# Performance work log

Measured on AMD Instinct MI355X. Metric: run time of the kernel, lower is better.

Reference implementation:

```python
import jax, jax.numpy as jnp
import numpy as np

GRID, RC, RD, FEAT, HID, PE = 300, 48, 16, 27, 128, 2
B, S = 4096, 128


def _grid_sample(img, grid):
    # img: (G,C,H,W); grid: (G,B,S,2) with (x=width, y=height) in [-1,1]
    # bilinear, align_corners=True (matches torch F.grid_sample defaults used here)
    G, C, H, W = img.shape
    x = (grid[..., 0] + 1.0) * 0.5 * (W - 1)  # (G,B,S)
    y = (grid[..., 1] + 1.0) * 0.5 * (H - 1)
    x0f, y0f = jnp.floor(x), jnp.floor(y)
    x0 = jnp.clip(x0f, 0, W - 1).astype(jnp.int32)
    y0 = jnp.clip(y0f, 0, H - 1).astype(jnp.int32)
    x1 = jnp.clip(x0 + 1, 0, W - 1)
    y1 = jnp.clip(y0 + 1, 0, H - 1)
    wx = (x - x0f)[:, None]  # (G,1,B,S)
    wy = (y - y0f)[:, None]

    def gather(im, yi, xi):  # im (C,H,W), yi/xi (B,S) -> (C,B,S)
        return im[:, yi, xi]

    g = jax.vmap(gather)
    v00 = g(img, y0, x0)
    v01 = g(img, y0, x1)
    v10 = g(img, y1, x0)
    v11 = g(img, y1, x1)
    return (v00 * (1 - wy) * (1 - wx) + v01 * (1 - wy) * wx
            + v10 * wy * (1 - wx) + v11 * wy * wx)  # (G,C,B,S)


def _vm(vectors, matrices, pos):
    # pos: (B,S,3) -> (B,S,3*R)
    b, s = pos.shape[0], pos.shape[1]
    mat_coord = jnp.stack([jnp.stack([pos[..., (i + 1) % 3], pos[..., (i + 2) % 3]], -1)
                           for i in range(3)], 0)  # (3,B,S,2)
    zero = jnp.zeros_like(pos[..., 0])
    vec_coord = jnp.stack([jnp.stack([pos[..., i], zero], -1) for i in range(3)], 0)
    m = _grid_sample(matrices, mat_coord)  # (3,R,B,S)
    v = _grid_sample(vectors, vec_coord)   # (3,R,B,S)
    return (m * v).transpose(2, 3, 0, 1).reshape(b, s, -1)


_COEFFS = (2.0 ** np.linspace(0.0, PE - 1, PE)) * np.pi  # [pi, 2pi]


def _pe(x):
    parts = []
    for c in _COEFFS:
        parts.append(jnp.sin(c * x))
        parts.append(jnp.cos(c * x))
    return jnp.concatenate(parts, -1)


def setup_inputs() -> dict:
    key = jax.random.key(0)
    ks = jax.random.split(key, 12)
    x = jax.random.uniform(ks[0], (B, S, 6), dtype=jnp.float32) * 2.0 - 1.0
    vmc_vec = jax.random.normal(ks[1], (3, RC, GRID, 1), dtype=jnp.float32) * 0.1
    vmc_mat = jax.random.normal(ks[2], (3, RC, GRID, GRID), dtype=jnp.float32) * 0.1
    vmd_vec = jax.random.normal(ks[3], (3, RD, GRID, 1), dtype=jnp.float32) * 0.1
    vmd_mat = jax.random.normal(ks[4], (3, RD, GRID, GRID), dtype=jnp.float32) * 0.1
    feat_w = jax.random.normal(ks[5], (FEAT, 3 * RC), dtype=jnp.float32) / np.sqrt(3 * RC)
    din = (1 + 2 * PE) * (3 + FEAT)  # 150
    w1 = jax.random.normal(ks[6], (HID, din), dtype=jnp.float32) / np.sqrt(din)
    b1 = jnp.zeros((HID,), jnp.float32)
    w2 = jax.random.normal(ks[7], (HID, HID), dtype=jnp.float32) / np.sqrt(HID)
    b2 = jnp.zeros((HID,), jnp.float32)
    w3 = jax.random.normal(ks[8], (3, HID), dtype=jnp.float32) / np.sqrt(HID)
    b3 = jnp.zeros((3,), jnp.float32)
    return {"x": x, "vmc_vec": vmc_vec, "vmc_mat": vmc_mat, "vmd_vec": vmd_vec,
            "vmd_mat": vmd_mat, "feat_w": feat_w, "w1": w1, "b1": b1,
            "w2": w2, "b2": b2, "w3": w3, "b3": b3}


def reference(x, vmc_vec, vmc_mat, vmd_vec, vmd_mat, feat_w, w1, b1, w2, b2, w3, b3):
    pos = x[..., :3]
    dirn = x[..., 3:]
    feature = jnp.einsum('bsk,fk->bsf', _vm(vmc_vec, vmc_mat, pos), feat_w)  # (B,S,27)
    mlp_in = jnp.concatenate([feature, dirn, _pe(feature), _pe(dirn)], -1)  # (B,S,150)
    h = jax.nn.relu(jnp.einsum('bsi,hi->bsh', mlp_in, w1) + b1)
    h = jax.nn.relu(jnp.einsum('bsi,hi->bsh', h, w2) + b2)
    color = jax.nn.sigmoid(jnp.einsum('bsi,oi->bso', h, w3) + b3)  # (B,S,3)
    density = jax.nn.relu(jnp.sum(_vm(vmd_vec, vmd_mat, pos), -1, keepdims=True))
    return jnp.concatenate([color, density], -1)  # (B,S,4)
```

## Files before the change

kernel.cpp:

```cpp
#include <hip/hip_runtime.h>
#include <stdint.h>

typedef unsigned int u32;
typedef _Float16 f16;
typedef __attribute__((ext_vector_type(8))) _Float16 f16x8;
typedef __attribute__((ext_vector_type(4))) float f32x4;
typedef __attribute__((ext_vector_type(2))) float f32x2;

#define XMS 168
#define HS  136

#define WOFF_WEFF 0u
#define WOFF_W1SW 10240u
#define WOFF_W2SW 51200u
#define WOFF_W3SW 83968u
#define WOFF_VD   88064u
#define WOFF_TM   131072u
#define WS_NEED   17411072u

#define TBL_SCALE 64.0f
#define TBL_INV   (1.0f/64.0f)

__global__ void prep_k(const float* __restrict__ feat_w,
                       const float* __restrict__ vmc_vec,
                       const float* __restrict__ vmd_vec,
                       const float* __restrict__ w1,
                       const float* __restrict__ w2,
                       const float* __restrict__ w3,
                       f16* __restrict__ Weff, f16* __restrict__ W1sw,
                       f16* __restrict__ W2sw, f16* __restrict__ W3sw,
                       float* __restrict__ vd)
{
  const int N_WEFF = 5120, N_W1 = 20480, N_W2 = 16384, N_W3 = 2048, N_VD = 48;
  const int total = N_WEFF + N_W1 + N_W2 + N_W3 + N_VD;
  for (int t = blockIdx.x*blockDim.x + threadIdx.x; t < total; t += gridDim.x*blockDim.x){
    if (t < N_WEFF){
      int kb = t >> 10, n = (t >> 5) & 31, kk = t & 31, k = kb*32 + kk;
      float v = 0.f;
      if (n < 27 && k < 144)
        v = feat_w[n*144 + k] * 0.5f*(vmc_vec[k*300+149] + vmc_vec[k*300+150]) * TBL_INV;
      Weff[t] = (f16)v;
    } else if (t < N_WEFF + N_W1){
      int u = t - N_WEFF;
      int kb = u >> 12, n = (u >> 5) & 127, kk = u & 31, k = kb*32 + kk;
      W1sw[u] = (f16)((k < 150) ? w1[n*150 + k] : 0.f);
    } else if (t < N_WEFF + N_W1 + N_W2){
      int u = t - N_WEFF - N_W1;
      int kb = u >> 12, n = (u >> 5) & 127, kk = u & 31, k = kb*32 + kk;
      W2sw[u] = (f16)w2[n*128 + k];
    } else if (t < N_WEFF + N_W1 + N_W2 + N_W3){
      int u = t - N_WEFF - N_W1 - N_W2;
      int kb = u >> 9, n = (u >> 5) & 15, kk = u & 31, k = kb*32 + kk;
      W3sw[u] = (f16)((n < 3) ? w3[n*128 + k] : 0.f);
    } else {
      int k = t - N_WEFF - N_W1 - N_W2 - N_W3;
      vd[k] = 0.5f*(vmd_vec[k*300+149] + vmd_vec[k*300+150]) * TBL_INV;
    }
  }
}

__global__ void pack_feat_k(const float* __restrict__ src, u32* __restrict__ dst)
{
  __shared__ float tile[48*304];
  int i = blockIdx.x / 300, y = blockIdx.x % 300;
  const float* sp = src + (size_t)i*48*90000 + (size_t)y*300;
  for (int t = threadIdx.x; t < 48*300; t += 256){
    int r = t / 300, x = t - r*300;
    tile[r*304 + x] = sp[(size_t)r*90000 + x] * TBL_SCALE;
  }
  __syncthreads();
  u32* dp = dst + (size_t)(i*300 + y)*300*16;
  for (int t = threadIdx.x; t < 300*12; t += 256){
    int x = t / 12, cg = t - x*12;
    int c = cg*4;
    u32 v = __builtin_amdgcn_cvt_pk_fp8_f32(tile[c*304+x],     tile[(c+1)*304+x], 0, false);
    v     = __builtin_amdgcn_cvt_pk_fp8_f32(tile[(c+2)*304+x], tile[(c+3)*304+x], v, true);
    dp[x*16 + cg] = v;
  }
}

__global__ void pack_dens_k(const float* __restrict__ src, u32* __restrict__ dst)
{
  __shared__ float tile[16*304];
  int i = blockIdx.x / 300, y = blockIdx.x % 300;
  const float* sp = src + (size_t)i*16*90000 + (size_t)y*300;
  for (int t = threadIdx.x; t < 16*300; t += 256){
    int r = t / 300, x = t - r*300;
    tile[r*304 + x] = sp[(size_t)r*90000 + x] * TBL_SCALE;
  }
  __syncthreads();
  u32* dp = dst + (size_t)(i*300 + y)*300*16;
  for (int t = threadIdx.x; t < 300*4; t += 256){
    int x = t / 4, cg = t - x*4;
    int c = cg*4;
    u32 v = __builtin_amdgcn_cvt_pk_fp8_f32(tile[c*304+x],     tile[(c+1)*304+x], 0, false);
    v     = __builtin_amdgcn_cvt_pk_fp8_f32(tile[(c+2)*304+x], tile[(c+3)*304+x], v, true);
    dp[x*16 + 12 + cg] = v;
  }
}

__device__ __forceinline__ void decode16(uint4 q, float* o){
  f32x2 t;
  t = __builtin_amdgcn_cvt_pk_f32_fp8(q.x, false); o[0]=t[0];  o[1]=t[1];
  t = __builtin_amdgcn_cvt_pk_f32_fp8(q.x, true ); o[2]=t[0];  o[3]=t[1];
  t = __builtin_amdgcn_cvt_pk_f32_fp8(q.y, false); o[4]=t[0];  o[5]=t[1];
  t = __builtin_amdgcn_cvt_pk_f32_fp8(q.y, true ); o[6]=t[0];  o[7]=t[1];
  t = __builtin_amdgcn_cvt_pk_f32_fp8(q.z, false); o[8]=t[0];  o[9]=t[1];
  t = __builtin_amdgcn_cvt_pk_f32_fp8(q.z, true ); o[10]=t[0]; o[11]=t[1];
  t = __builtin_amdgcn_cvt_pk_f32_fp8(q.w, false); o[12]=t[0]; o[13]=t[1];
  t = __builtin_amdgcn_cvt_pk_f32_fp8(q.w, true ); o[14]=t[0]; o[15]=t[1];
}

__global__ __launch_bounds__(256, 3)
void main_k(const float* __restrict__ xin,
            const f16* __restrict__ WeffSw, const f16* __restrict__ W1sw,
            const f16* __restrict__ W2sw, const f16* __restrict__ W3sw,
            const float* __restrict__ vd,
            const uint4* __restrict__ Tm,
            const float* __restrict__ b1v, const float* __restrict__ b2v,
            const float* __restrict__ b3v, float* __restrict__ out)
{
  __shared__ __align__(16) f16 bufA[64*XMS];
  __shared__ __align__(16) f16 bufB[64*XMS];
  __shared__ float dLds[192];

  const int tid = threadIdx.x;
  const int l = tid & 63;
  const int w = tid >> 6;
  const size_t nidx = (size_t)blockIdx.x*64 + l;

  const float* xp = xin + nidx*6;
  float p0 = xp[0], p1 = xp[1], p2 = xp[2];
  float d0 = xp[3], d1 = xp[4], d2 = xp[5];

  if (w < 3){
    float cx = (w==0)? p1 : ((w==1)? p2 : p0);
    float cy = (w==0)? p2 : ((w==1)? p0 : p1);
    float fx = (cx+1.f)*0.5f*299.f, fy = (cy+1.f)*0.5f*299.f;
    float x0f = floorf(fx), y0f = floorf(fy);
    int x0 = min(max((int)x0f,0),299), y0 = min(max((int)y0f,0),299);
    int x1 = min(x0+1,299), y1 = min(y0+1,299);
    float wx = fx-x0f, wy = fy-y0f;
    float w11 = wx*wy, w10 = wy - w11, w01 = wx - w11, w00 = 1.f - wx - wy + w11;

    const uint4* Tb = Tm + (size_t)w*90000*4;
    const uint4* r00 = Tb + (size_t)(y0*300+x0)*4;
    const uint4* r01 = Tb + (size_t)(y0*300+x1)*4;
    const uint4* r10 = Tb + (size_t)(y1*300+x0)*4;
    const uint4* r11 = Tb + (size_t)(y1*300+x1)*4;
    uint4 qa[4], qb[4], qc[4], qd[4];
#pragma unroll
    for (int c4=0;c4<4;++c4){ qa[c4]=r00[c4]; qb[c4]=r01[c4]; qc[c4]=r10[c4]; qd[c4]=r11[c4]; }

    float vdw[16];
#pragma unroll
    for (int j=0;j<16;++j) vdw[j] = vd[w*16 + j];

    f16* dstrow = bufA + l*XMS + w*48;
    float dacc = 0.f;
#pragma unroll
    for (int c4=0;c4<4;++c4){
      float A[16],B[16],C[16],D[16];
      decode16(qa[c4],A); decode16(qb[c4],B); decode16(qc[c4],C); decode16(qd[c4],D);
      if (c4 < 3){
        f16x8 o0, o1;
#pragma unroll
        for (int j=0;j<8;++j)
          o0[j] = (f16)(w00*A[j] + w01*B[j] + w10*C[j] + w11*D[j]);
#pragma unroll
        for (int j=0;j<8;++j)
          o1[j] = (f16)(w00*A[8+j] + w01*B[8+j] + w10*C[8+j] + w11*D[8+j]);
        *(f16x8*)(dstrow + c4*16)     = o0;
        *(f16x8*)(dstrow + c4*16 + 8) = o1;
      } else {
#pragma unroll
        for (int j=0;j<16;++j)
          dacc += (w00*A[j] + w01*B[j] + w10*C[j] + w11*D[j]) * vdw[j];
      }
    }
    dLds[w*64 + l] = dacc;
  } else {
    f16x8 z = 0;
    *(f16x8*)(bufA + l*XMS + 144) = z;
    *(f16x8*)(bufA + l*XMS + 152) = z;
  }
  __syncthreads();

  const int tr = l & 15;
  const int ko = (l >> 4) * 8;

  {
    if (w == 3){
      float ds = dLds[l] + dLds[64 + l] + dLds[128 + l];
      out[nidx*4 + 3] = fmaxf(ds, 0.f);
    }
    f32x4 fa0 = {0.f,0.f,0.f,0.f}, fa1 = {0.f,0.f,0.f,0.f};
    const f16* Arow = bufA + (w*16 + tr)*XMS + ko;
#pragma unroll
    for (int kb=0; kb<5; ++kb){
      f16x8 a  = *(const f16x8*)(Arow + kb*32);
      f16x8 b0 = *(const f16x8*)(WeffSw + (size_t)(kb*32 + tr)*32 + ko);
      f16x8 b1 = *(const f16x8*)(WeffSw + (size_t)(kb*32 + 16 + tr)*32 + ko);
      fa0 = __builtin_amdgcn_mfma_f32_16x16x32_f16(a, b0, fa0, 0,0,0);
      fa1 = __builtin_amdgcn_mfma_f32_16x16x32_f16(a, b1, fa1, 0,0,0);
    }
    const int sbase = w*16 + (l>>4)*4;
#pragma unroll
    for (int nb=0; nb<2; ++nb){
      int f = nb*16 + tr;
      if (f < 27){
#pragma unroll
        for (int r=0;r<4;++r){
          float fv = nb ? fa1[r] : fa0[r];
          f16* Xr = bufB + (sbase + r)*XMS;
          Xr[f] = (f16)fv;
          float a1 = 3.14159265358979f*fv;
          float a2 = 6.28318530717959f*fv;
          Xr[30+f]  = (f16)__sinf(a1);
          Xr[57+f]  = (f16)__cosf(a1);
          Xr[84+f]  = (f16)__sinf(a2);
          Xr[111+f] = (f16)__cosf(a2);
        }
      }
    }
    if (w == 0){
      f16* Xr = bufB + l*XMS;
      Xr[27]=(f16)d0; Xr[28]=(f16)d1; Xr[29]=(f16)d2;
      float dv[3]={d0,d1,d2};
#pragma unroll
      for (int j=0;j<3;++j){
        float a1=3.14159265358979f*dv[j], a2=6.28318530717959f*dv[j];
        Xr[138+j]=(f16)__sinf(a1);
        Xr[141+j]=(f16)__cosf(a1);
        Xr[144+j]=(f16)__sinf(a2);
        Xr[147+j]=(f16)__cosf(a2);
      }
#pragma unroll
      for (int j=150;j<160;++j) Xr[j]=(f16)0.f;
    }
  }
  __syncthreads();

  {
    f32x4 acc[4][2];
#pragma unroll
    for (int m=0;m<4;++m){ acc[m][0]=(f32x4){0.f,0.f,0.f,0.f}; acc[m][1]=(f32x4){0.f,0.f,0.f,0.f}; }
    const int n0 = w*32 + tr;
#pragma unroll
    for (int kb=0; kb<5; ++kb){
      f16x8 b0 = *(const f16x8*)(W1sw + (size_t)(kb*128 + n0)*32 + ko);
      f16x8 b1 = *(const f16x8*)(W1sw + (size_t)(kb*128 + n0 + 16)*32 + ko);
#pragma unroll
      for (int m=0;m<4;++m){
        f16x8 a = *(const f16x8*)(bufB + (m*16 + tr)*XMS + kb*32 + ko);
        acc[m][0] = __builtin_amdgcn_mfma_f32_16x16x32_f16(a, b0, acc[m][0], 0,0,0);
        acc[m][1] = __builtin_amdgcn_mfma_f32_16x16x32_f16(a, b1, acc[m][1], 0,0,0);
      }
    }
    float bb0 = b1v[n0], bb1 = b1v[n0+16];
    f16* H1 = bufA;
#pragma unroll
    for (int m=0;m<4;++m){
#pragma unroll
      for (int r=0;r<4;++r){
        int ss = m*16 + (l>>4)*4 + r;
        H1[ss*HS + n0]      = (f16)fmaxf(acc[m][0][r] + bb0, 0.f);
        H1[ss*HS + n0 + 16] = (f16)fmaxf(acc[m][1][r] + bb1, 0.f);
      }
    }
  }
  __syncthreads();

  {
    f32x4 acc[4][2];
#pragma unroll
    for (int m=0;m<4;++m){ acc[m][0]=(f32x4){0.f,0.f,0.f,0.f}; acc[m][1]=(f32x4){0.f,0.f,0.f,0.f}; }
    const int n0 = w*32 + tr;
    const f16* H1 = bufA;
#pragma unroll
    for (int kb=0; kb<4; ++kb){
      f16x8 b0 = *(const f16x8*)(W2sw + (size_t)(kb*128 + n0)*32 + ko);
      f16x8 b1 = *(const f16x8*)(W2sw + (size_t)(kb*128 + n0 + 16)*32 + ko);
#pragma unroll
      for (int m=0;m<4;++m){
        f16x8 a = *(const f16x8*)(H1 + (m*16 + tr)*HS + kb*32 + ko);
        acc[m][0] = __builtin_amdgcn_mfma_f32_16x16x32_f16(a, b0, acc[m][0], 0,0,0);
        acc[m][1] = __builtin_amdgcn_mfma_f32_16x16x32_f16(a, b1, acc[m][1], 0,0,0);
      }
    }
    float bb0 = b2v[n0], bb1 = b2v[n0+16];
    f16* H2 = bufB;
#pragma unroll
    for (int m=0;m<4;++m){
#pragma unroll
      for (int r=0;r<4;++r){
        int ss = m*16 + (l>>4)*4 + r;
        H2[ss*HS + n0]      = (f16)fmaxf(acc[m][0][r] + bb0, 0.f);
        H2[ss*HS + n0 + 16] = (f16)fmaxf(acc[m][1][r] + bb1, 0.f);
      }
    }
  }
  __syncthreads();

  {
    f32x4 acc = {0.f,0.f,0.f,0.f};
    const f16* H2 = bufB;
#pragma unroll
    for (int kb=0; kb<4; ++kb){
      f16x8 a = *(const f16x8*)(H2 + (w*16 + tr)*HS + kb*32 + ko);
      f16x8 b = *(const f16x8*)(W3sw + (size_t)(kb*16 + tr)*32 + ko);
      acc = __builtin_amdgcn_mfma_f32_16x16x32_f16(a, b, acc, 0,0,0);
    }
    if (tr < 3){
      float bb = b3v[tr];
#pragma unroll
      for (int r=0;r<4;++r){
        int ss = w*16 + (l>>4)*4 + r;
        float c = acc[r] + bb;
        out[((size_t)blockIdx.x*64 + ss)*4 + tr] = 1.f/(1.f + __expf(-c));
      }
    }
  }
}

extern "C" void kernel_launch(void* const* d_in, const int* in_sizes, int n_in,
                              void* d_out, int out_size, void* d_ws, size_t ws_size,
                              hipStream_t stream)
{
  const float* xin     = (const float*)d_in[0];
  const float* vmc_vec = (const float*)d_in[1];
  const float* vmc_mat = (const float*)d_in[2];
  const float* vmd_vec = (const float*)d_in[3];
  const float* vmd_mat = (const float*)d_in[4];
  const float* feat_w  = (const float*)d_in[5];
  const float* w1      = (const float*)d_in[6];
  const float* b1      = (const float*)d_in[7];
  const float* w2      = (const float*)d_in[8];
  const float* b2      = (const float*)d_in[9];
  const float* w3      = (const float*)d_in[10];
  const float* b3      = (const float*)d_in[11];
  float* out = (float*)d_out;

  char* ws = (char*)d_ws;
  f16*   Weff = (f16*)(ws + WOFF_WEFF);
  f16*   W1sw = (f16*)(ws + WOFF_W1SW);
  f16*   W2sw = (f16*)(ws + WOFF_W2SW);
  f16*   W3sw = (f16*)(ws + WOFF_W3SW);
  float* vd   = (float*)(ws + WOFF_VD);
  u32*   Tm   = (u32*)(ws + WOFF_TM);

  prep_k<<<64, 256, 0, stream>>>(feat_w, vmc_vec, vmd_vec, w1, w2, w3,
                                 Weff, W1sw, W2sw, W3sw, vd);
  pack_feat_k<<<900, 256, 0, stream>>>(vmc_mat, Tm);
  pack_dens_k<<<900, 256, 0, stream>>>(vmd_mat, Tm);

  main_k<<<8192, 256, 0, stream>>>(xin, Weff, W1sw, W2sw, W3sw, vd,
                                   (const uint4*)Tm, b1, b2, b3, out);
}
```

Measured before the change: 222.2 us.

## Shrink LDS footprint by reusing one buffer and raise occupancy to four blocks

Merges the two large shared-memory staging buffers into one input buffer plus a smaller hidden-activation buffer. The MLP input is now built in place over the gathered features, which is safe because each wave only reads and writes its own 16 rows. Together with launch bounds raised to 4 blocks per CU, this aims to fit more blocks per CU so more latency from the random table gathers is hidden. Direction loads and their encoding are spread across all four waves instead of one, and a scheduling barrier orders the in-place overwrite. The tighter register budget risks spills.

```diff
diff --git a/kernel.cpp b/kernel.cpp
--- a/kernel.cpp
+++ b/kernel.cpp
@@ -111,7 +111,7 @@
   t = __builtin_amdgcn_cvt_pk_f32_fp8(q.w, true ); o[14]=t[0]; o[15]=t[1];
 }
 
-__global__ __launch_bounds__(256, 3)
+__global__ __launch_bounds__(256, 4)
 void main_k(const float* __restrict__ xin,
             const f16* __restrict__ WeffSw, const f16* __restrict__ W1sw,
             const f16* __restrict__ W2sw, const f16* __restrict__ W3sw,
@@ -120,8 +120,8 @@
             const float* __restrict__ b1v, const float* __restrict__ b2v,
             const float* __restrict__ b3v, float* __restrict__ out)
 {
-  __shared__ __align__(16) f16 bufA[64*XMS];
-  __shared__ __align__(16) f16 bufB[64*XMS];
+  __shared__ __align__(16) f16 buf[64*XMS];
+  __shared__ __align__(16) f16 bufH[64*HS];
   __shared__ float dLds[192];
 
   const int tid = threadIdx.x;
@@ -131,7 +131,12 @@
 
   const float* xp = xin + nidx*6;
   float p0 = xp[0], p1 = xp[1], p2 = xp[2];
-  float d0 = xp[3], d1 = xp[4], d2 = xp[5];
+
+  float dd0=0.f, dd1=0.f, dd2=0.f;
+  if (l < 16){
+    const float* dp = xin + ((size_t)blockIdx.x*64 + w*16 + l)*6 + 3;
+    dd0 = dp[0]; dd1 = dp[1]; dd2 = dp[2];
+  }
 
   if (w < 3){
     float cx = (w==0)? p1 : ((w==1)? p2 : p0);
@@ -156,7 +161,7 @@
 #pragma unroll
     for (int j=0;j<16;++j) vdw[j] = vd[w*16 + j];
 
-    f16* dstrow = bufA + l*XMS + w*48;
+    f16* dstrow = buf + l*XMS + w*48;
     float dacc = 0.f;
 #pragma unroll
     for (int c4=0;c4<4;++c4){
@@ -181,8 +186,8 @@
     dLds[w*64 + l] = dacc;
   } else {
     f16x8 z = 0;
-    *(f16x8*)(bufA + l*XMS + 144) = z;
-    *(f16x8*)(bufA + l*XMS + 152) = z;
+    *(f16x8*)(buf + l*XMS + 144) = z;
+    *(f16x8*)(buf + l*XMS + 152) = z;
   }
   __syncthreads();
 
@@ -195,7 +200,7 @@
       out[nidx*4 + 3] = fmaxf(ds, 0.f);
     }
     f32x4 fa0 = {0.f,0.f,0.f,0.f}, fa1 = {0.f,0.f,0.f,0.f};
-    const f16* Arow = bufA + (w*16 + tr)*XMS + ko;
+    const f16* Arow = buf + (w*16 + tr)*XMS + ko;
 #pragma unroll
     for (int kb=0; kb<5; ++kb){
       f16x8 a  = *(const f16x8*)(Arow + kb*32);
@@ -204,6 +209,9 @@
       fa0 = __builtin_amdgcn_mfma_f32_16x16x32_f16(a, b0, fa0, 0,0,0);
       fa1 = __builtin_amdgcn_mfma_f32_16x16x32_f16(a, b1, fa1, 0,0,0);
     }
+    __builtin_amdgcn_sched_barrier(0);
+    asm volatile("" : "+v"(dd0), "+v"(dd1), "+v"(dd2) : "v"(fa0[0]));
+
     const int sbase = w*16 + (l>>4)*4;
 #pragma unroll
     for (int nb=0; nb<2; ++nb){
@@ -212,7 +220,7 @@
 #pragma unroll
         for (int r=0;r<4;++r){
           float fv = nb ? fa1[r] : fa0[r];
-          f16* Xr = bufB + (sbase + r)*XMS;
+          f16* Xr = buf + (sbase + r)*XMS;
           Xr[f] = (f16)fv;
           float a1 = 3.14159265358979f*fv;
           float a2 = 6.28318530717959f*fv;
@@ -223,10 +231,10 @@
         }
       }
     }
-    if (w == 0){
-      f16* Xr = bufB + l*XMS;
-      Xr[27]=(f16)d0; Xr[28]=(f16)d1; Xr[29]=(f16)d2;
-      float dv[3]={d0,d1,d2};
+    if (l < 16){
+      f16* Xr = buf + (w*16 + l)*XMS;
+      Xr[27]=(f16)dd0; Xr[28]=(f16)dd1; Xr[29]=(f16)dd2;
+      float dv[3]={dd0,dd1,dd2};
 #pragma unroll
       for (int j=0;j<3;++j){
         float a1=3.14159265358979f*dv[j], a2=6.28318530717959f*dv[j];
@@ -235,8 +243,6 @@
         Xr[144+j]=(f16)__sinf(a2);
         Xr[147+j]=(f16)__cosf(a2);
       }
-#pragma unroll
-      for (int j=150;j<160;++j) Xr[j]=(f16)0.f;
     }
   }
   __syncthreads();
@@ -252,20 +258,19 @@
       f16x8 b1 = *(const f16x8*)(W1sw + (size_t)(kb*128 + n0 + 16)*32 + ko);
 #pragma unroll
       for (int m=0;m<4;++m){
-        f16x8 a = *(const f16x8*)(bufB + (m*16 + tr)*XMS + kb*32 + ko);
+        f16x8 a = *(const f16x8*)(buf + (m*16 + tr)*XMS + kb*32 + ko);
         acc[m][0] = __builtin_amdgcn_mfma_f32_16x16x32_f16(a, b0, acc[m][0], 0,0,0);
         acc[m][1] = __builtin_amdgcn_mfma_f32_16x16x32_f16(a, b1, acc[m][1], 0,0,0);
       }
     }
     float bb0 = b1v[n0], bb1 = b1v[n0+16];
-    f16* H1 = bufA;
 #pragma unroll
     for (int m=0;m<4;++m){
 #pragma unroll
       for (int r=0;r<4;++r){
         int ss = m*16 + (l>>4)*4 + r;
-        H1[ss*HS + n0]      = (f16)fmaxf(acc[m][0][r] + bb0, 0.f);
-        H1[ss*HS + n0 + 16] = (f16)fmaxf(acc[m][1][r] + bb1, 0.f);
+        bufH[ss*HS + n0]      = (f16)fmaxf(acc[m][0][r] + bb0, 0.f);
+        bufH[ss*HS + n0 + 16] = (f16)fmaxf(acc[m][1][r] + bb1, 0.f);
       }
     }
   }
@@ -276,27 +281,25 @@
 #pragma unroll
     for (int m=0;m<4;++m){ acc[m][0]=(f32x4){0.f,0.f,0.f,0.f}; acc[m][1]=(f32x4){0.f,0.f,0.f,0.f}; }
     const int n0 = w*32 + tr;
-    const f16* H1 = bufA;
 #pragma unroll
     for (int kb=0; kb<4; ++kb){
       f16x8 b0 = *(const f16x8*)(W2sw + (size_t)(kb*128 + n0)*32 + ko);
       f16x8 b1 = *(const f16x8*)(W2sw + (size_t)(kb*128 + n0 + 16)*32 + ko);
 #pragma unroll
       for (int m=0;m<4;++m){
-        f16x8 a = *(const f16x8*)(H1 + (m*16 + tr)*HS + kb*32 + ko);
+        f16x8 a = *(const f16x8*)(bufH + (m*16 + tr)*HS + kb*32 + ko);
         acc[m][0] = __builtin_amdgcn_mfma_f32_16x16x32_f16(a, b0, acc[m][0], 0,0,0);
         acc[m][1] = __builtin_amdgcn_mfma_f32_16x16x32_f16(a, b1, acc[m][1], 0,0,0);
       }
     }
     float bb0 = b2v[n0], bb1 = b2v[n0+16];
-    f16* H2 = bufB;
 #pragma unroll
     for (int m=0;m<4;++m){
 #pragma unroll
       for (int r=0;r<4;++r){
         int ss = m*16 + (l>>4)*4 + r;
-        H2[ss*HS + n0]      = (f16)fmaxf(acc[m][0][r] + bb0, 0.f);
-        H2[ss*HS + n0 + 16] = (f16)fmaxf(acc[m][1][r] + bb1, 0.f);
+        buf[ss*HS + n0]      = (f16)fmaxf(acc[m][0][r] + bb0, 0.f);
+        buf[ss*HS + n0 + 16] = (f16)fmaxf(acc[m][1][r] + bb1, 0.f);
       }
     }
   }
@@ -304,10 +307,9 @@
 
   {
     f32x4 acc = {0.f,0.f,0.f,0.f};
-    const f16* H2 = bufB;
 #pragma unroll
     for (int kb=0; kb<4; ++kb){
-      f16x8 a = *(const f16x8*)(H2 + (w*16 + tr)*HS + kb*32 + ko);
+      f16x8 a = *(const f16x8*)(buf + (w*16 + tr)*HS + kb*32 + ko);
       f16x8 b = *(const f16x8*)(W3sw + (size_t)(kb*16 + tr)*32 + ko);
       acc = __builtin_amdgcn_mfma_f32_16x16x32_f16(a, b, acc, 0,0,0);
     }
```

Result: faster. 183.7 us (-17.3%).
